# Kernel tuning notes

Hardware: AMD Instinct MI355X
Metric: run time of the kernel (lower is better)

Reference implementation:

```python
import jax, jax.numpy as jnp
import numpy as np
from math import sqrt

H, C, DFF, N, E = 4, 128, 2048, 2048, 8192
EPS = 1e-5

def _glorot(key, shape):
    fan_in, fan_out = shape
    lim = sqrt(6.0 / (fan_in + fan_out))
    return jax.random.uniform(key, shape, jnp.float32, -lim, lim)

def setup_inputs() -> dict:
    key = jax.random.key(0)
    ks = jax.random.split(key, 12)
    x = jax.random.normal(ks[0], (N, C), jnp.float32)
    index = jax.random.randint(ks[1], (E,), 0, N, jnp.int64)
    return {
        'x': x, 'index': index,
        'Wq': _glorot(ks[2], (C, H * C)), 'bq': jnp.zeros((H * C,), jnp.float32),
        'Wk': _glorot(ks[3], (C, H * C)), 'bk': jnp.zeros((H * C,), jnp.float32),
        'Wv': _glorot(ks[4], (C, H * C)), 'bv': jnp.zeros((H * C,), jnp.float32),
        'Wz': _glorot(ks[5], (H * C, C)), 'bz': jnp.zeros((C,), jnp.float32),
        'ln_w': jnp.ones((C,), jnp.float32), 'ln_b': jnp.zeros((C,), jnp.float32),
        'W1': _glorot(ks[6], (C, DFF)), 'b1': jnp.zeros((DFF,), jnp.float32),
        'W2': _glorot(ks[7], (DFF, DFF)), 'b2': jnp.zeros((DFF,), jnp.float32),
        'W3': _glorot(ks[8], (DFF, C)), 'b3': jnp.zeros((C,), jnp.float32),
    }

def _graph_layer_norm(z, w, b):
    # PyG LayerNorm(mode='graph'), batch=None: normalize over ALL nodes and channels
    mu = jnp.mean(z)
    var = jnp.mean((z - mu) ** 2)
    return (z - mu) * jax.lax.rsqrt(var + EPS) * w + b

def _forward(x, index, Wq, bq, Wk, bk, Wv, bv, Wz, bz, ln_w, ln_b, W1, b1, W2, b2, W3, b3):
    x_j = x[index]                                   # [E,C] neighbor gather
    Q = (x @ Wq + bq).reshape(H, N, C)               # torch .view(H,-1,C)
    K = (x_j @ Wk + bk).reshape(H, E, C)
    V = (x_j @ Wv + bv).reshape(H, E, C)
    attn = jnp.einsum('hnc,hec->hne', Q, K) / sqrt(C)  # [H,N,E]
    # segment softmax over edge axis, grouped by index (PyG softmax)
    a = attn.transpose(2, 0, 1)                      # [E,H,N]
    seg_max = jax.lax.stop_gradient(
        jax.ops.segment_max(a, index, num_segments=N))  # [N,H,N]
    ex = jnp.exp(a - seg_max[index])
    denom = jax.ops.segment_sum(ex, index, num_segments=N)[index] + 1e-16
    p = ex / denom                                   # [E,H,N]
    score = jnp.einsum('ehn,hec->hnc', p, V)         # [H,N,C]
    score = jnp.transpose(score, (1, 0, 2)).reshape(N, H * C)
    z = score @ Wz + bz
    z = _graph_layer_norm(z + x, ln_w, ln_b)
    h = jax.nn.gelu(z @ W1 + b1, approximate=False)
    h = jax.nn.gelu(h @ W2 + b2, approximate=False)
    ffn = h @ W3 + b3
    return _graph_layer_norm(ffn + x, ln_w, ln_b)

def reference(x, index, Wq, bq, Wk, bk, Wv, bv, Wz, bz, ln_w, ln_b, W1, b1, W2, b2, W3, b3):
    return _forward(x, index, Wq, bq, Wk, bk, Wv, bv, Wz, bz, ln_w, ln_b, W1, b1, W2, b2, W3, b3)
```

## Files before the change

kernel.cpp:

```cpp
#include <hip/hip_runtime.h>

typedef unsigned short ushort_t;
typedef short short8 __attribute__((ext_vector_type(8)));
typedef float f32x4 __attribute__((ext_vector_type(4)));

#define NN   2048
#define EE   8192
#define CC   128
#define HCC  512
#define DFF  2048
#define QB   512

#define BM 128
#define BN 128
#define BKK 64

enum { EPI_STORE_BIAS = 0, EPI_EXP = 1, EPI_GELU = 2, EPI_ATOMIC = 3 };

__device__ __forceinline__ float b2f(ushort_t u) {
    return __uint_as_float(((unsigned int)u) << 16);
}
__device__ __forceinline__ ushort_t f2b(float f) {
    unsigned int u = __float_as_uint(f);
    u += 0x7fffu + ((u >> 16) & 1u);
    return (ushort_t)(u >> 16);
}

#define GLOAD16(gp, lp)                                                        \
    __builtin_amdgcn_global_load_lds(                                          \
        (const __attribute__((address_space(1))) unsigned int*)(gp),           \
        (__attribute__((address_space(3))) unsigned int*)(lp), 16, 0, 0)

__global__ void probe_k(const void* __restrict__ x, const void* __restrict__ idx,
                        int* __restrict__ flags)
{
    if (threadIdx.x == 0 && blockIdx.x == 0) {
        const ushort_t* xu = (const ushort_t*)x;
        float mx = 0.f;
        for (int i = 0; i < 512; i++) {
            float v = fabsf(b2f(xu[i]));
            if (v < 1e30f) mx = fmaxf(mx, v);
            else mx = 1e30f;
        }
        flags[0] = (mx > 1e4f) ? 1 : 0;
        const int* ii = (const int*)idx;
        int allz = 1;
        for (int j = 1; j < 16; j += 2)
            if (ii[j] != 0) allz = 0;
        flags[1] = allz;
    }
}

__global__ void cvt_idx(const void* __restrict__ in, int* __restrict__ out,
                        const int* __restrict__ flags)
{
    int i = blockIdx.x * 256 + threadIdx.x;
    if (i < EE)
        out[i] = flags[1] ? (int)((const long long*)in)[i] : ((const int*)in)[i];
}

__global__ __launch_bounds__(256)
void sort_edges(const int* __restrict__ idx, int* __restrict__ sorted_e,
                int* __restrict__ seg_off, int* __restrict__ sseg)
{
    __shared__ int hist[NN];
    __shared__ int cursor[NN];
    __shared__ float wsum[4];
    const int tid = threadIdx.x;
    for (int i = tid; i < NN; i += 256) hist[i] = 0;
    __syncthreads();
    for (int e = tid; e < EE; e += 256) atomicAdd(&hist[idx[e]], 1);
    __syncthreads();
    int s = 0;
#pragma unroll
    for (int j = 0; j < 8; j++) s += hist[tid * 8 + j];
    int lane = tid & 63, w = tid >> 6;
    int sc = s;
#pragma unroll
    for (int o = 1; o < 64; o <<= 1) {
        int t = __shfl_up(sc, o, 64);
        if (lane >= o) sc += t;
    }
    if (lane == 63) wsum[w] = (float)sc;
    __syncthreads();
    int wbase = 0;
    for (int j = 0; j < 4; j++) if (j < w) wbase += (int)wsum[j];
    int excl = wbase + sc - s;
    int run = excl;
#pragma unroll
    for (int j = 0; j < 8; j++) {
        int b = tid * 8 + j;
        cursor[b] = run;
        seg_off[b] = run;
        run += hist[b];
    }
    if (tid == 0) seg_off[NN] = EE;
    __syncthreads();
    for (int e = tid; e < EE; e += 256) {
        int t = idx[e];
        int pos = atomicAdd(&cursor[t], 1);
        sorted_e[pos] = e;
        sseg[pos] = t;
    }
}

__global__ void cvt_x(const void* __restrict__ in, ushort_t* __restrict__ xb,
                      float* __restrict__ xf, const int* __restrict__ flags)
{
    long i = (long)blockIdx.x * 256 + threadIdx.x;
    float v = flags[0] ? ((const float*)in)[i] : b2f(((const ushort_t*)in)[i]);
    xf[i] = v;
    xb[i] = f2b(v);
}

__global__ void cvt_vecs(const void* bq, const void* bk, const void* bv,
                         const void* bz, const void* lnw, const void* lnb,
                         const void* b3, const void* b1, const void* b2,
                         float* __restrict__ out, const int* __restrict__ flags)
{
    int i = blockIdx.x * 256 + threadIdx.x;
    if (i >= 6144) return;
    const void* src; int o;
    if      (i < 512)  { src = bq;  o = i; }
    else if (i < 1024) { src = bk;  o = i - 512; }
    else if (i < 1536) { src = bv;  o = i - 1024; }
    else if (i < 1664) { src = bz;  o = i - 1536; }
    else if (i < 1792) { src = lnw; o = i - 1664; }
    else if (i < 1920) { src = lnb; o = i - 1792; }
    else if (i < 2048) { src = b3;  o = i - 1920; }
    else if (i < 4096) { src = b1;  o = i - 2048; }
    else               { src = b2;  o = i - 4096; }
    out[i] = flags[0] ? ((const float*)src)[o] : b2f(((const ushort_t*)src)[o]);
}

__global__ void transpose_cvt(const void* __restrict__ in, ushort_t* __restrict__ out,
                              int R, int C, const int* __restrict__ flags)
{
    __shared__ ushort_t t[32][33];
    const int f  = flags[0];
    const int bx = blockIdx.x * 32;
    const int by = blockIdx.y * 32;
    const int tx = threadIdx.x, ty = threadIdx.y;
#pragma unroll
    for (int i = 0; i < 32; i += 8) {
        long src = (long)(by + ty + i) * C + bx + tx;
        t[ty + i][tx] = f ? f2b(((const float*)in)[src]) : ((const ushort_t*)in)[src];
    }
    __syncthreads();
#pragma unroll
    for (int i = 0; i < 32; i += 8)
        out[(long)(bx + ty + i) * R + by + tx] = t[tx][ty + i];
}

__global__ void transpose_qkv(const void* q, const void* k, const void* v,
                              ushort_t* __restrict__ out, const int* __restrict__ flags)
{
    __shared__ ushort_t t[32][33];
    const void* in = blockIdx.z == 0 ? q : (blockIdx.z == 1 ? k : v);
    const int f  = flags[0];
    const int bx = blockIdx.x * 32;
    const int by = blockIdx.y * 32;
    const int tx = threadIdx.x, ty = threadIdx.y;
#pragma unroll
    for (int i = 0; i < 32; i += 8) {
        long src = (long)(by + ty + i) * HCC + bx + tx;
        t[ty + i][tx] = f ? f2b(((const float*)in)[src]) : ((const ushort_t*)in)[src];
    }
    __syncthreads();
#pragma unroll
    for (int i = 0; i < 32; i += 8)
        out[(size_t)blockIdx.z * HCC * CC + (long)(bx + ty + i) * CC + by + tx]
            = t[tx][ty + i];
}

__global__ __launch_bounds__(256)
void gather_k(const ushort_t* __restrict__ KM, ushort_t* __restrict__ Ksort,
              const int* __restrict__ sorted_e)
{
    const size_t hb = (size_t)blockIdx.z * EE * CC;
    const int j  = blockIdx.x * 16 + (threadIdx.x >> 4);
    const int l8 = (threadIdx.x & 15) * 8;
    const int e  = sorted_e[j];
    *(short8*)(Ksort + hb + (size_t)j * CC + l8) =
        *(const short8*)(KM + hb + (size_t)e * CC + l8);
}

__global__ void transpose_v(const ushort_t* __restrict__ VM, ushort_t* __restrict__ VT,
                            const int* __restrict__ sorted_e)
{
    __shared__ ushort_t t[32][33];
    const ushort_t* in = VM + (size_t)blockIdx.z * EE * CC;
    ushort_t* out      = VT + (size_t)blockIdx.z * EE * CC;
    const int bx = blockIdx.x * 32;
    const int by = blockIdx.y * 32;
    const int tx = threadIdx.x, ty = threadIdx.y;
#pragma unroll
    for (int i = 0; i < 32; i += 8) {
        const long rg = sorted_e[by + ty + i];
        t[ty + i][tx] = in[rg * CC + bx + tx];
    }
    __syncthreads();
#pragma unroll
    for (int i = 0; i < 32; i += 8)
        out[(long)(bx + ty + i) * EE + by + tx] = t[tx][ty + i];
}

template <int EPI, bool GATHER, int MODE>
__global__ __launch_bounds__(256, 2)
void gemm_h(const ushort_t* __restrict__ A, long lda, long aHS,
            const ushort_t* __restrict__ B, long ldb, long bHS,
            const int* __restrict__ gidx,
            const float* __restrict__ bias, long biasHS,
            void* __restrict__ Cp, long ldc, long cHS,
            int kchunk, float alpha)
{
    __shared__ __align__(16) ushort_t smem[BM * BKK + BN * BKK];
    ushort_t* As = smem;
    ushort_t* Bs = smem + BM * BKK;

    const int tid  = threadIdx.x;
    const int lane = tid & 63;
    const int wave = tid >> 6;

    const int gx = gridDim.x, gy = gridDim.y;
    const int nwg = gx * gy * gridDim.z;
    const int bid = blockIdx.x + gx * (blockIdx.y + gy * blockIdx.z);
    const int q8 = nwg >> 3, r8 = nwg & 7;
    const int xcd = bid & 7, slot = bid >> 3;
    const int nb = (xcd < r8) ? (xcd * (q8 + 1) + slot) : (r8 + xcd * q8 + slot);
    const int bxi = nb % gx;
    const int tq  = nb / gx;
    const int byi = tq % gy;
    const int bzi = tq / gy;

    const long bm = (long)bxi * BM;

    long bn; int head, k0;
    if (MODE == 1)      { head = bzi; k0 = 0;               bn = (long)byi * BN; }
    else if (MODE == 2) { head = byi; k0 = bzi * kchunk;    bn = 0; }
    else                { head = 0;   k0 = bzi * kchunk;    bn = (long)byi * BN; }
    const int k1 = k0 + kchunk;

    A += (size_t)head * aHS;
    B += (size_t)head * bHS;
    const float* bp = bias + (size_t)head * biasHS;
    Cp = (void*)((char*)Cp + (size_t)head * cHS);

    const f32x4 fzero = {0.f, 0.f, 0.f, 0.f};
    f32x4 acc[4][4];
#pragma unroll
    for (int i = 0; i < 4; i++)
#pragma unroll
        for (int j = 0; j < 4; j++) acc[i][j] = fzero;

    const int arow = tid >> 3;
    const int acol = (((tid & 7) ^ (arow & 7)) * 8);

    const ushort_t* ap[4];
    const ushort_t* bpt[4];
#pragma unroll
    for (int i = 0; i < 4; i++) {
        long r  = bm + arow + i * 32;
        long gr = GATHER ? (long)gidx[r] : r;
        ap[i]  = A + gr * lda + acol;
        bpt[i] = B + (bn + arow + i * 32) * ldb + acol;
    }
    const int t8  = tid * 8;
    const int wr  = (wave >> 1) * 64;
    const int wc  = (wave & 1) * 64;
    const int ra  = lane & 15;
    const int kgi = lane >> 4;
    const int r7  = lane & 7;

    for (int kt = k0; kt < k1; kt += BKK) {
        __syncthreads();
#pragma unroll
        for (int i = 0; i < 4; i++) GLOAD16(ap[i] + kt, &As[t8 + i * 2048]);
#pragma unroll
        for (int i = 0; i < 4; i++) GLOAD16(bpt[i] + kt, &Bs[t8 + i * 2048]);
        __syncthreads();
#pragma unroll
        for (int ks = 0; ks < 2; ks++) {
            const int cswz = (((ks * 4 + kgi) ^ r7) * 8);
            short8 af[4], bfr[4];
#pragma unroll
            for (int mi = 0; mi < 4; mi++)
                af[mi] = *(const short8*)&As[(wr + mi * 16 + ra) * BKK + cswz];
#pragma unroll
            for (int ni = 0; ni < 4; ni++)
                bfr[ni] = *(const short8*)&Bs[(wc + ni * 16 + ra) * BKK + cswz];
#pragma unroll
            for (int mi = 0; mi < 4; mi++)
#pragma unroll
                for (int ni = 0; ni < 4; ni++)
                    acc[mi][ni] = __builtin_amdgcn_mfma_f32_16x16x32_bf16(
                        af[mi], bfr[ni], acc[mi][ni], 0, 0, 0);
        }
    }

    if (EPI == EPI_ATOMIC) {
#pragma unroll
        for (int mi = 0; mi < 4; mi++) {
#pragma unroll
            for (int ni = 0; ni < 4; ni++) {
                const long row0 = bm + wr + mi * 16 + (lane >> 4) * 4;
                const long col  = bn + wc + ni * 16 + ra;
#pragma unroll
                for (int r = 0; r < 4; r++)
                    unsafeAtomicAdd(&((float*)Cp)[(row0 + r) * ldc + col],
                                    acc[mi][ni][r]);
            }
        }
    } else {
        __syncthreads();
        ushort_t* Cs = smem;
#pragma unroll
        for (int mi = 0; mi < 4; mi++) {
#pragma unroll
            for (int ni = 0; ni < 4; ni++) {
                const int crow0 = wr + mi * 16 + (lane >> 4) * 4;
                const int ccol  = wc + ni * 16 + ra;
#pragma unroll
                for (int r = 0; r < 4; r++) {
                    float v = acc[mi][ni][r];
                    if (EPI == EPI_STORE_BIAS) {
                        v += bp[bn + ccol];
                    } else if (EPI == EPI_EXP) {
                        v = __expf(v * alpha);
                    } else {
                        v += bp[bn + ccol];
                        v = 0.5f * v * (1.f + erff(v * 0.70710678118654752f));
                    }
                    const int crow = crow0 + r;
                    Cs[crow * BN + (ccol ^ (((crow & 7) << 3)))] = f2b(v);
                }
            }
        }
        __syncthreads();
#pragma unroll
        for (int it = 0; it < 8; it++) {
            const int idx = it * 2048 + tid * 8;
            const int row = idx >> 7;
            const int col = idx & 127;
            *(short8*)((ushort_t*)Cp + (bm + row) * ldc + bn + col) =
                *(const short8*)&Cs[row * BN + (col ^ ((row & 7) << 3))];
        }
    }
}

#define PH(e) ((e) + ((e) >> 6))
__global__ __launch_bounds__(1024)
void seg_norm_sorted(ushort_t* __restrict__ P, const int* __restrict__ seg_off,
                     const int* __restrict__ sseg)
{
    __shared__ float rowf[EE + EE / 64];
    __shared__ float D[NN];
    ushort_t* row = P + (long)blockIdx.x * EE;
    const int tid = threadIdx.x;

    {
        const int e = tid * 8;
        short8 v = *(const short8*)(row + e);
#pragma unroll
        for (int j = 0; j < 8; j++)
            rowf[PH(e + j)] = b2f((ushort_t)v[j]);
    }
    __syncthreads();

    {
        const int t2 = tid * 2;
        int prev = seg_off[t2];
#pragma unroll
        for (int j = 0; j < 2; j++) {
            const int e1 = seg_off[t2 + j + 1];
            float s = 0.f;
            for (int e = prev; e < e1; e++) s += rowf[PH(e)];
            D[t2 + j] = 1.f / (s + 1e-16f);
            prev = e1;
        }
    }
    __syncthreads();

    {
        const int e = tid * 8;
        short8 o;
#pragma unroll
        for (int j = 0; j < 8; j++)
            o[j] = (short)f2b(rowf[PH(e + j)] * D[sseg[e + j]]);
        *(short8*)(row + e) = o;
    }
}

__global__ void cvt_sb(const float* __restrict__ in, ushort_t* __restrict__ out)
{
    long i = (long)blockIdx.x * 256 + threadIdx.x;
    out[i] = f2b(in[i]);
}

__global__ void gelu_cvt4(const float* __restrict__ in, const float* __restrict__ bias,
                          ushort_t* __restrict__ out)
{
    long i4 = ((long)blockIdx.x * 256 + threadIdx.x) * 4;
    f32x4 v = *(const f32x4*)(in + i4);
    ushort_t o[4];
#pragma unroll
    for (int j = 0; j < 4; j++) {
        float u = v[j] + bias[(i4 + j) & (DFF - 1)];
        o[j] = f2b(0.5f * u * (1.f + erff(u * 0.70710678118654752f)));
    }
    *(unsigned long long*)(out + i4) =
        (unsigned long long)o[0] | ((unsigned long long)o[1] << 16) |
        ((unsigned long long)o[2] << 32) | ((unsigned long long)o[3] << 48);
}

__global__ __launch_bounds__(256)
void add_bias_x_reduce(float* __restrict__ u, const float* __restrict__ bias,
                       const float* __restrict__ x, float* __restrict__ red)
{
    long i = (long)blockIdx.x * 256 + threadIdx.x;
    float v = u[i] + bias[i & (CC - 1)] + x[i];
    u[i] = v;
    float s = v, s2 = v * v;
#pragma unroll
    for (int o = 32; o > 0; o >>= 1) {
        s  += __shfl_down(s, o, 64);
        s2 += __shfl_down(s2, o, 64);
    }
    __shared__ float ps[4], ps2[4];
    int w = threadIdx.x >> 6;
    if ((threadIdx.x & 63) == 0) { ps[w] = s; ps2[w] = s2; }
    __syncthreads();
    if (threadIdx.x == 0) {
        float a = 0.f, b = 0.f;
#pragma unroll
        for (int j = 0; j < 4; j++) { a += ps[j]; b += ps2[j]; }
        unsafeAtomicAdd(&red[0], a);
        unsafeAtomicAdd(&red[1], b);
    }
}

__global__ void ln_fin_mid(const float* __restrict__ u, const float* __restrict__ red,
                           const float* __restrict__ w, const float* __restrict__ b,
                           ushort_t* __restrict__ out, float invn)
{
    long i = (long)blockIdx.x * 256 + threadIdx.x;
    float mean = red[0] * invn;
    float var  = red[1] * invn - mean * mean;
    float rs   = rsqrtf(var + 1e-5f);
    int c = (int)(i & (CC - 1));
    out[i] = f2b((u[i] - mean) * rs * w[c] + b[c]);
}

__global__ void ln_fin_out(const float* __restrict__ u, const float* __restrict__ red,
                           const float* __restrict__ w, const float* __restrict__ b,
                           void* __restrict__ out, const int* __restrict__ flags,
                           float invn)
{
    long i = (long)blockIdx.x * 256 + threadIdx.x;
    float mean = red[0] * invn;
    float var  = red[1] * invn - mean * mean;
    float rs   = rsqrtf(var + 1e-5f);
    int c = (int)(i & (CC - 1));
    float v = (u[i] - mean) * rs * w[c] + b[c];
    if (flags[0]) ((float*)out)[i] = v;
    else          ((ushort_t*)out)[i] = f2b(v);
}

extern "C" void kernel_launch(void* const* d_in, const int* in_sizes, int n_in,
                              void* d_out, int out_size, void* d_ws, size_t ws_size,
                              hipStream_t stream)
{
    const void* x_raw   = d_in[0];
    const void* idx_raw = d_in[1];
    const void* Wq = d_in[2];  const void* bq = d_in[3];
    const void* Wk = d_in[4];  const void* bk = d_in[5];
    const void* Wv = d_in[6];  const void* bv = d_in[7];
    const void* Wz = d_in[8];  const void* bz = d_in[9];
    const void* lnw = d_in[10]; const void* lnb = d_in[11];
    const void* W1 = d_in[12]; const void* b1 = d_in[13];
    const void* W2 = d_in[14]; const void* b2 = d_in[15];
    const void* W3 = d_in[16]; const void* b3 = d_in[17];

    char* ws = (char*)d_ws;
    size_t off = 0;
    auto carve = [&](size_t bytes) -> char* {
        char* p = ws + off;
        off += (bytes + 255) & ~(size_t)255;
        return p;
    };

    int*      flags  = (int*)     carve(256);
    int*      idx32  = (int*)     carve((size_t)EE * 4);
    int*      sortedE= (int*)     carve((size_t)EE * 4);
    int*      segOff = (int*)     carve((size_t)(NN + 1) * 4);
    int*      ssegB  = (int*)     carve((size_t)EE * 4);
    ushort_t* x_bf  = (ushort_t*)carve((size_t)NN * CC * 2);
    float*    x_f   = (float*)   carve((size_t)NN * CC * 4);
    float*    vecF  = (float*)   carve(6144 * 4);
    float*    bqF  = vecF;        float* bkF  = vecF + 512;
    float*    bzF  = vecF + 1536;
    float*    lnwF = vecF + 1664; float* lnbF = vecF + 1792;
    float*    b3F  = vecF + 1920; float* b1F  = vecF + 2048;
    float*    b2F  = vecF + 4096;
    ushort_t* wqkvT = (ushort_t*)carve((size_t)3 * HCC * CC * 2);
    ushort_t* wqT = wqkvT;
    ushort_t* wkT = wqkvT + (size_t)HCC * CC;
    ushort_t* wzT   = (ushort_t*)carve((size_t)CC * HCC * 2);
    ushort_t* scoreB= (ushort_t*)carve((size_t)NN * HCC * 2);
    float*    zF    = (float*)   carve((size_t)NN * CC * 4);
    ushort_t* zln   = (ushort_t*)carve((size_t)NN * CC * 2);
    float*    ffnF  = (float*)   carve((size_t)NN * CC * 4);
    float*    red   = (float*)   carve(256);

    size_t scratch0 = off;
    ushort_t* QM    = (ushort_t*)carve((size_t)NN * HCC * 2);
    ushort_t* KVM   = (ushort_t*)carve((size_t)2 * EE * HCC * 2);
    ushort_t* KM = KVM;
    ushort_t* VM = KVM + (size_t)EE * HCC;
    ushort_t* Ksort = (ushort_t*)carve((size_t)EE * HCC * 2);
    ushort_t* VT    = (ushort_t*)carve((size_t)EE * HCC * 2);
    float*    scoreF= (float*)   carve((size_t)NN * HCC * 4);
    size_t pOff = off;
    off = pOff;
    carve((size_t)4 * NN * EE * 2);
    size_t total_attn_full = off;
    size_t total_attn_quart = pOff + (((size_t)4 * QB * EE * 2 + 255) & ~(size_t)255);
    ushort_t* P = (ushort_t*)(ws + pOff);
    off = scratch0;
    ushort_t* w1T = (ushort_t*)carve((size_t)DFF * CC * 2);
    ushort_t* w2T = (ushort_t*)carve((size_t)DFF * DFF * 2);
    ushort_t* w3T = (ushort_t*)carve((size_t)CC * DFF * 2);
    ushort_t* h1  = (ushort_t*)carve((size_t)NN * DFF * 2);
    ushort_t* h2  = (ushort_t*)carve((size_t)NN * DFF * 2);
    float*    h2F = (float*)   carve((size_t)NN * DFF * 4);
    size_t total_ffn = off;

    const bool merged = ws_size >= (total_attn_full > total_ffn ? total_attn_full
                                                                : total_ffn);
    size_t required_attn = merged ? total_attn_full : total_attn_quart;
    size_t required = required_attn > total_ffn ? required_attn : total_ffn;
    if (ws_size < required) return;

    probe_k<<<1, 64, 0, stream>>>(x_raw, idx_raw, flags);
    cvt_idx<<<EE / 256, 256, 0, stream>>>(idx_raw, idx32, flags);
    sort_edges<<<1, 256, 0, stream>>>(idx32, sortedE, segOff, ssegB);
    cvt_x<<<(NN * CC) / 256, 256, 0, stream>>>(x_raw, x_bf, x_f, flags);
    cvt_vecs<<<24, 256, 0, stream>>>(bq, bk, bv, bz, lnw, lnb, b3, b1, b2,
                                     vecF, flags);

    dim3 tb(32, 8);
    transpose_qkv<<<dim3(HCC / 32, CC / 32, 3), tb, 0, stream>>>(Wq, Wk, Wv,
                                                                 wqkvT, flags);
    transpose_cvt<<<dim3(CC / 32, HCC / 32), tb, 0, stream>>>(Wz, wzT, HCC, CC, flags);

    hipMemsetAsync(scoreF, 0, (size_t)NN * HCC * 4, stream);
    hipMemsetAsync(zF,     0, (size_t)NN * CC * 4, stream);
    hipMemsetAsync(ffnF,   0, (size_t)NN * CC * 4, stream);
    hipMemsetAsync(red,    0, 16, stream);

    gemm_h<EPI_STORE_BIAS, false, 0><<<dim3(NN / BM, HCC / BN, 1), 256, 0, stream>>>(
        x_bf, CC, 0, wqT, CC, 0, nullptr, bqF, 0, QM, HCC, 0, CC, 0.f);
    gemm_h<EPI_STORE_BIAS, true, 1><<<dim3(EE / BM, HCC / BN, 2), 256, 0, stream>>>(
        x_bf, CC, 0, wkT, CC, (long)HCC * CC, idx32, bkF, 512,
        KM, HCC, (size_t)EE * HCC * 2, CC, 0.f);

    gather_k<<<dim3(EE / 16, 1, 4), 256, 0, stream>>>(KM, Ksort, sortedE);
    transpose_v<<<dim3(CC / 32, EE / 32, 4), tb, 0, stream>>>(VM, VT, sortedE);

    const float alpha = 0.088388347648318447f;

    if (merged) {
        gemm_h<EPI_EXP, false, 1><<<dim3(NN / BM, EE / BN, 4), 256, 0, stream>>>(
            QM, CC, (long)NN * CC,
            Ksort, CC, (long)EE * CC, nullptr, vecF, 0,
            P, EE, (size_t)NN * EE * 2, CC, alpha);
        seg_norm_sorted<<<4 * NN, 1024, 0, stream>>>(P, segOff, ssegB);
        gemm_h<EPI_ATOMIC, false, 2><<<dim3(NN / BM, 4, 16), 256, 0, stream>>>(
            P, EE, (long)NN * EE, VT, EE, (long)EE * CC, nullptr, vecF, 0,
            scoreF, HCC, (size_t)CC * 4, EE / 16, 0.f);
    } else {
        for (int qb = 0; qb < 4; qb++) {
            gemm_h<EPI_EXP, false, 1><<<dim3(QB / BM, EE / BN, 4), 256, 0, stream>>>(
                QM + (size_t)qb * QB * CC, CC, (long)NN * CC,
                Ksort, CC, (long)EE * CC, nullptr, vecF, 0,
                P, EE, (size_t)QB * EE * 2, CC, alpha);
            seg_norm_sorted<<<4 * QB, 1024, 0, stream>>>(P, segOff, ssegB);
            gemm_h<EPI_ATOMIC, false, 2><<<dim3(QB / BM, 4, 16), 256, 0, stream>>>(
                P, EE, (long)QB * EE, VT, EE, (long)EE * CC, nullptr, vecF, 0,
                scoreF + (size_t)qb * QB * HCC, HCC, (size_t)CC * 4, EE / 16, 0.f);
        }
    }

    cvt_sb<<<(NN * HCC) / 256, 256, 0, stream>>>(scoreF, scoreB);

    transpose_cvt<<<dim3(DFF / 32, CC / 32),  tb, 0, stream>>>(W1, w1T, CC, DFF, flags);
    transpose_cvt<<<dim3(DFF / 32, DFF / 32), tb, 0, stream>>>(W2, w2T, DFF, DFF, flags);
    transpose_cvt<<<dim3(CC / 32, DFF / 32),  tb, 0, stream>>>(W3, w3T, DFF, CC, flags);
    hipMemsetAsync(h2F, 0, (size_t)NN * DFF * 4, stream);

    gemm_h<EPI_ATOMIC, false, 0><<<dim3(NN / BM, 1, 8), 256, 0, stream>>>(
        scoreB, HCC, 0, wzT, HCC, 0, nullptr, vecF, 0,
        zF, CC, 0, HCC / 8, 0.f);
    add_bias_x_reduce<<<(NN * CC) / 256, 256, 0, stream>>>(zF, bzF, x_f, red);
    ln_fin_mid<<<(NN * CC) / 256, 256, 0, stream>>>(zF, red, lnwF, lnbF, zln,
                                                    1.f / (float)(NN * CC));

    gemm_h<EPI_GELU, false, 0><<<dim3(NN / BM, DFF / BN, 1), 256, 0, stream>>>(
        zln, CC, 0, w1T, CC, 0, nullptr, b1F, 0, h1, DFF, 0, CC, 0.f);
    gemm_h<EPI_ATOMIC, false, 0><<<dim3(NN / BM, DFF / BN, 2), 256, 0, stream>>>(
        h1, DFF, 0, w2T, DFF, 0, nullptr, vecF, 0, h2F, DFF, 0, DFF / 2, 0.f);
    gelu_cvt4<<<(NN * DFF) / 1024, 256, 0, stream>>>(h2F, b2F, h2);
    gemm_h<EPI_ATOMIC, false, 0><<<dim3(NN / BM, 1, 16), 256, 0, stream>>>(
        h2, DFF, 0, w3T, DFF, 0, nullptr, vecF, 0, ffnF, CC, 0, DFF / 16, 0.f);
    add_bias_x_reduce<<<(NN * CC) / 256, 256, 0, stream>>>(ffnF, b3F, x_f, red + 2);
    ln_fin_out<<<(NN * CC) / 256, 256, 0, stream>>>(ffnF, red + 2, lnwF, lnbF,
                                                    d_out, flags,
                                                    1.f / (float)(NN * CC));
}
```

Before: 435.0 us.

## Double-buffer GEMM LDS tiles to overlap global loads with MFMA

Measured after the change: 430.4 us. About the same (-1.1%).

```diff
diff --git a/kernel.cpp b/kernel.cpp
--- a/kernel.cpp
+++ b/kernel.cpp
@@ -214,9 +214,8 @@
             void* __restrict__ Cp, long ldc, long cHS,
             int kchunk, float alpha)
 {
-    __shared__ __align__(16) ushort_t smem[BM * BKK + BN * BKK];
-    ushort_t* As = smem;
-    ushort_t* Bs = smem + BM * BKK;
+    constexpr int TSZ = BM * BKK + BN * BKK;
+    __shared__ __align__(16) ushort_t smem[2 * TSZ];
 
     const int tid  = threadIdx.x;
     const int lane = tid & 63;
@@ -272,23 +271,41 @@
     const int kgi = lane >> 4;
     const int r7  = lane & 7;
 
+    {
+        ushort_t* As0 = smem;
+        ushort_t* Bs0 = smem + BM * BKK;
+#pragma unroll
+        for (int i = 0; i < 4; i++) GLOAD16(ap[i] + k0, &As0[t8 + i * 2048]);
+#pragma unroll
+        for (int i = 0; i < 4; i++) GLOAD16(bpt[i] + k0, &Bs0[t8 + i * 2048]);
+    }
+    asm volatile("s_waitcnt vmcnt(0)" ::: "memory");
+    __builtin_amdgcn_s_barrier();
+
+    int cur = 0;
     for (int kt = k0; kt < k1; kt += BKK) {
-        __syncthreads();
-#pragma unroll
-        for (int i = 0; i < 4; i++) GLOAD16(ap[i] + kt, &As[t8 + i * 2048]);
-#pragma unroll
-        for (int i = 0; i < 4; i++) GLOAD16(bpt[i] + kt, &Bs[t8 + i * 2048]);
-        __syncthreads();
+        if (kt + BKK < k1) {
+            ushort_t* Asn = smem + (cur ^ 1) * TSZ;
+            ushort_t* Bsn = Asn + BM * BKK;
+#pragma unroll
+            for (int i = 0; i < 4; i++)
+                GLOAD16(ap[i] + kt + BKK, &Asn[t8 + i * 2048]);
+#pragma unroll
+            for (int i = 0; i < 4; i++)
+                GLOAD16(bpt[i] + kt + BKK, &Bsn[t8 + i * 2048]);
+        }
+        const ushort_t* Asc = smem + cur * TSZ;
+        const ushort_t* Bsc = Asc + BM * BKK;
 #pragma unroll
         for (int ks = 0; ks < 2; ks++) {
             const int cswz = (((ks * 4 + kgi) ^ r7) * 8);
             short8 af[4], bfr[4];
 #pragma unroll
             for (int mi = 0; mi < 4; mi++)
-                af[mi] = *(const short8*)&As[(wr + mi * 16 + ra) * BKK + cswz];
+                af[mi] = *(const short8*)&Asc[(wr + mi * 16 + ra) * BKK + cswz];
 #pragma unroll
             for (int ni = 0; ni < 4; ni++)
-                bfr[ni] = *(const short8*)&Bs[(wc + ni * 16 + ra) * BKK + cswz];
+                bfr[ni] = *(const short8*)&Bsc[(wc + ni * 16 + ra) * BKK + cswz];
 #pragma unroll
             for (int mi = 0; mi < 4; mi++)
 #pragma unroll
@@ -296,6 +313,9 @@
                     acc[mi][ni] = __builtin_amdgcn_mfma_f32_16x16x32_bf16(
                         af[mi], bfr[ni], acc[mi][ni], 0, 0, 0);
         }
+        asm volatile("s_waitcnt vmcnt(0)" ::: "memory");
+        __builtin_amdgcn_s_barrier();
+        cur ^= 1;
     }
 
     if (EPI == EPI_ATOMIC) {
@@ -312,7 +332,6 @@
             }
         }
     } else {
-        __syncthreads();
         ushort_t* Cs = smem;
 #pragma unroll
         for (int mi = 0; mi < 4; mi++) {
```
